# Kernel optimization log

Measured on AMD Instinct MI355X. Metric: run time of the kernel, lower is better.

Reference implementation:

```python
import jax, jax.numpy as jnp
import numpy as np

N_NODES = 100000
N_EDGES = 1600000
D_IN = 128
D_HID = 128
N_CLS = 40


def setup_inputs() -> dict:
    key = jax.random.key(0)
    ks = jax.random.split(key, 8)
    x = jax.random.normal(ks[0], (N_NODES, D_IN), dtype=jnp.float32)
    edge_index = jax.random.randint(ks[1], (2, N_EDGES), 0, N_NODES, dtype=jnp.int64)
    s = 1.0 / np.sqrt(D_IN)
    W1_l = jax.random.normal(ks[2], (D_IN, D_HID), dtype=jnp.float32) * s
    W1_r = jax.random.normal(ks[3], (D_IN, D_HID), dtype=jnp.float32) * s
    b1 = jnp.zeros((D_HID,), dtype=jnp.float32)
    s2 = 1.0 / np.sqrt(D_HID)
    W2_l = jax.random.normal(ks[4], (D_HID, N_CLS), dtype=jnp.float32) * s2
    W2_r = jax.random.normal(ks[5], (D_HID, N_CLS), dtype=jnp.float32) * s2
    b2 = jnp.zeros((N_CLS,), dtype=jnp.float32)
    return {"x": x, "edge_index": edge_index, "W1_l": W1_l, "W1_r": W1_r,
            "b1": b1, "W2_l": W2_l, "W2_r": W2_r, "b2": b2}


def _sage_conv(x, src, dst, Wl, Wr, b):
    # mean-aggregate neighbor features (PyG SAGEConv, aggr='mean')
    n = x.shape[0]
    agg = jax.ops.segment_sum(x[src], dst, num_segments=n)           # [N, d]
    deg = jax.ops.segment_sum(jnp.ones_like(dst, dtype=x.dtype), dst, num_segments=n)
    mean = agg / jnp.maximum(deg, 1.0)[:, None]
    # lin_l(mean) + bias + lin_r(x_root)  (lin_r has no bias in PyG)
    return mean @ Wl + b + x @ Wr


def reference(x, edge_index, W1_l, W1_r, b1, W2_l, W2_r, b2):
    src, dst = edge_index[0], edge_index[1]
    h = jax.nn.relu(_sage_conv(x, src, dst, W1_l, W1_r, b1))
    # F.dropout(training=...) is identity in eval mode (deterministic reference)
    out = _sage_conv(h, src, dst, W2_l, W2_r, b2)
    return jax.nn.softmax(out, axis=1)
```

## Files before the change

### kernel.cpp

```cpp
#include <hip/hip_runtime.h>

#define DIM 128
#define NCLS 40
#define CPAD 64
#define NBIN 256
#define BINSH 9
#define CHUNK 4096

typedef unsigned short ushort_t;
typedef __attribute__((ext_vector_type(8))) short bf16x8;
typedef __attribute__((ext_vector_type(4))) float f32x4;
typedef __attribute__((ext_vector_type(4))) unsigned uint4a;

__device__ __forceinline__ ushort_t f2b(float f) {
    union { float f; unsigned u; } v; v.f = f;
    unsigned r = v.u + 0x7FFFu + ((v.u >> 16) & 1u);
    return (ushort_t)(r >> 16);
}

__device__ __forceinline__ float b2f(ushort_t b) {
    union { unsigned u; float f; } v; v.u = ((unsigned)b) << 16;
    return v.f;
}

__device__ __forceinline__ void acc_fp8x4(float4& a, int w) {
    a.x += __builtin_amdgcn_cvt_f32_fp8(w, 0);
    a.y += __builtin_amdgcn_cvt_f32_fp8(w, 1);
    a.z += __builtin_amdgcn_cvt_f32_fp8(w, 2);
    a.w += __builtin_amdgcn_cvt_f32_fp8(w, 3);
}

__device__ __forceinline__ void acc_pair(float& a, float& b, unsigned u) {
    union { unsigned x; float f; } lo, hi;
    lo.x = u << 16;
    hi.x = u & 0xFFFF0000u;
    a += lo.f;
    b += hi.f;
}

__global__ __launch_bounds__(256) void prep_kernel(
    const float* __restrict__ x, ushort_t* __restrict__ xbf, unsigned* __restrict__ xq,
    const float* __restrict__ W1r, const float* __restrict__ W1l, ushort_t* __restrict__ Wp,
    const float* __restrict__ W2l, ushort_t* __restrict__ Wp2,
    int* __restrict__ binCnt, int* __restrict__ binCtr, int n4, int cb)
{
    const int b = blockIdx.x;
    if (b < cb) {
        int i = b * 256 + threadIdx.x;
        if (i >= n4) return;
        f32x4 v = __builtin_nontemporal_load(((const f32x4*)x) + i);
        ushort4 o;
        o.x = f2b(v.x); o.y = f2b(v.y); o.z = f2b(v.z); o.w = f2b(v.w);
        ((ushort4*)xbf)[i] = o;
        int p = __builtin_amdgcn_cvt_pk_fp8_f32(v.x, v.y, 0, false);
        p = __builtin_amdgcn_cvt_pk_fp8_f32(v.z, v.w, p, true);
        xq[i] = (unsigned)p;
    } else if (b < cb + 128) {
        int o = (b - cb) * 256 + threadIdx.x;
        int j    = o & 7;
        int lane = (o >> 3) & 63;
        int t    = (o >> 9) & 7;
        int kc   = o >> 12;
        int k = kc * 32 + (lane >> 4) * 8 + j;
        int nn = t * 16 + (lane & 15);
        float v = (k < DIM) ? W1r[k * DIM + nn] : W1l[(k - DIM) * DIM + nn];
        Wp[o] = f2b(v);
    } else if (b < cb + 152) {
        int o = (b - cb - 128) * 256 + threadIdx.x;
        int j    = o & 7;
        int lane = (o >> 3) & 63;
        int rem  = o >> 9;
        int t    = rem % 3;
        int kc   = rem / 3;
        int k  = kc * 32 + (lane >> 4) * 8 + j;
        int nn = t * 16 + (lane & 15);
        Wp2[o] = (nn < NCLS) ? f2b(W2l[k * NCLS + nn]) : (ushort_t)0;
    } else {
        binCnt[threadIdx.x] = 0;
        binCtr[threadIdx.x] = 0;
    }
}


__global__ __launch_bounds__(256) void bincount_kernel(const int* __restrict__ dst,
                                                       int* __restrict__ binCnt, int E) {
    __shared__ int hist[NBIN];
    hist[threadIdx.x] = 0;
    __syncthreads();
    const int tid = blockIdx.x * 256 + threadIdx.x;
    const int stride = gridDim.x * 256;
    for (int e = tid; e < E; e += stride)
        atomicAdd(&hist[__builtin_nontemporal_load(dst + e) >> BINSH], 1);
    __syncthreads();
    if (hist[threadIdx.x]) atomicAdd(&binCnt[threadIdx.x], hist[threadIdx.x]);
}

__global__ __launch_bounds__(256) void binscatter_kernel(
    const int* __restrict__ src, const int* __restrict__ dst,
    const int* __restrict__ binCnt, int* __restrict__ binCtr,
    unsigned* __restrict__ pairs, int E)
{
    __shared__ int ss[CHUNK];
    __shared__ int sd[CHUNK];
    __shared__ int excl[NBIN];
    __shared__ int hist[NBIN];
    __shared__ int base[NBIN];
    __shared__ int cnt[NBIN];
    const int t = threadIdx.x;
    excl[t] = binCnt[t];
    __syncthreads();
    for (int off = 1; off < NBIN; off <<= 1) {
        int v = (t >= off) ? excl[t - off] : 0;
        __syncthreads();
        excl[t] += v;
        __syncthreads();
    }
    const int mybase = (t == 0) ? 0 : excl[t - 1];
    __syncthreads();
    excl[t] = mybase;
    __syncthreads();
    const int nchunk = (E + CHUNK - 1) / CHUNK;
    for (int c = blockIdx.x; c < nchunk; c += gridDim.x) {
        const int e0 = c * CHUNK;
        const int m = min(CHUNK, E - e0);
        for (int i = t; i < m; i += 256) {
            ss[i] = __builtin_nontemporal_load(src + e0 + i);
            sd[i] = __builtin_nontemporal_load(dst + e0 + i);
        }
        hist[t] = 0;
        cnt[t] = 0;
        __syncthreads();
        for (int i = t; i < m; i += 256)
            atomicAdd(&hist[sd[i] >> BINSH], 1);
        __syncthreads();
        base[t] = hist[t] ? (excl[t] + atomicAdd(&binCtr[t], hist[t])) : 0;
        __syncthreads();
        for (int i = t; i < m; i += 256) {
            int d = sd[i];
            int b = d >> BINSH;
            int off = base[b] + atomicAdd(&cnt[b], 1);
            pairs[off] = ((unsigned)(d & ((1 << BINSH) - 1)) << 17) | (unsigned)ss[i];
        }
        __syncthreads();
    }
}

__global__ __launch_bounds__(256) void bincsr_kernel(
    const unsigned* __restrict__ pairs, const int* __restrict__ binCnt,
    int* __restrict__ row_ptr, int* __restrict__ eidx, int n, int E)
{
    __shared__ int bs[NBIN];
    __shared__ int deg[512];
    __shared__ int sc[512];
    __shared__ int cnt[512];
    const int b  = blockIdx.x;
    const int t = threadIdx.x;
    bs[t] = binCnt[t];
    __syncthreads();
    for (int off = 1; off < NBIN; off <<= 1) {
        int v = (t >= off) ? bs[t - off] : 0;
        __syncthreads();
        bs[t] += v;
        __syncthreads();
    }
    const int lo = (b == 0) ? 0 : bs[b - 1];
    const int hi = bs[b];
    const int nlo = b << BINSH;
    deg[t] = 0; deg[t + 256] = 0;
    cnt[t] = 0; cnt[t + 256] = 0;
    __syncthreads();
    for (int e = lo + t; e < hi; e += 256)
        atomicAdd(&deg[pairs[e] >> 17], 1);
    __syncthreads();
    sc[t] = deg[t];
    sc[t + 256] = deg[t + 256];
    __syncthreads();
    for (int off = 1; off < 512; off <<= 1) {
        int v0 = (t >= off) ? sc[t - off] : 0;
        int v1 = sc[t + 256 - off];
        __syncthreads();
        sc[t] += v0;
        sc[t + 256] += v1;
        __syncthreads();
    }
    {
        int node0 = nlo + t;
        int node1 = nlo + t + 256;
        if (node0 < n) row_ptr[node0] = lo + sc[t] - deg[t];
        if (node1 < n) row_ptr[node1] = lo + sc[t + 256] - deg[t + 256];
    }
    if (b == NBIN - 1 && t == 255) row_ptr[n] = E;
    for (int e = lo + t; e < hi; e += 256) {
        unsigned p = pairs[e];
        int dl = p >> 17;
        int slot = sc[dl] - deg[dl] + atomicAdd(&cnt[dl], 1);
        eidx[lo + slot] = (int)(p & 0x1FFFFu);
    }
}


__global__ __launch_bounds__(256) void gather128_kernel(
    const unsigned* __restrict__ xq, const int* __restrict__ row_ptr,
    const int* __restrict__ eidx, ushort_t* __restrict__ Bbf, int n)
{
    int t = blockIdx.x * 256 + threadIdx.x;
    int node = t >> 5;
    if (node >= n) return;
    int q = t & 31;
    int j  = row_ptr[node];
    int je = row_ptr[node + 1];
    const float id = 1.0f / fmaxf((float)(je - j), 1.0f);
    float4 acc = make_float4(0.f, 0.f, 0.f, 0.f);
    for (; j + 3 < je; j += 4) {
        int s0 = eidx[j], s1 = eidx[j + 1], s2 = eidx[j + 2], s3 = eidx[j + 3];
        int w0 = (int)xq[(size_t)s0 * 32 + q];
        int w1 = (int)xq[(size_t)s1 * 32 + q];
        int w2 = (int)xq[(size_t)s2 * 32 + q];
        int w3 = (int)xq[(size_t)s3 * 32 + q];
        acc_fp8x4(acc, w0); acc_fp8x4(acc, w1);
        acc_fp8x4(acc, w2); acc_fp8x4(acc, w3);
    }
    for (; j < je; ++j) {
        int s0 = eidx[j];
        acc_fp8x4(acc, (int)xq[(size_t)s0 * 32 + q]);
    }
    ushort4 o;
    o.x = f2b(acc.x * id); o.y = f2b(acc.y * id);
    o.z = f2b(acc.z * id); o.w = f2b(acc.w * id);
    ((ushort4*)(Bbf + (size_t)node * DIM))[q] = o;
}

__global__ __launch_bounds__(256) void mfma_gemm_kernel(
    const ushort_t* __restrict__ xbf, const ushort_t* __restrict__ mxbf,
    const ushort_t* __restrict__ Wp, const ushort_t* __restrict__ Wp2,
    const float* __restrict__ bias,
    ushort_t* __restrict__ Hbf, ushort_t* __restrict__ Cbf, int n)
{
    __shared__ ushort_t hl[4][16 * 136];
    const int wave = threadIdx.x >> 6;
    const int lane = threadIdx.x & 63;
    const int m16  = lane & 15;
    const int quad = lane >> 4;
    const int row0 = blockIdx.x * 64 + wave * 16;
    int arow = row0 + m16;
    if (arow >= n) arow = n - 1;
    f32x4 acc[8];
    #pragma unroll
    for (int t = 0; t < 8; ++t) acc[t] = (f32x4){0.f, 0.f, 0.f, 0.f};
    const ushort_t* __restrict__ xrow = xbf  + (size_t)arow * DIM;
    const ushort_t* __restrict__ mrow = mxbf + (size_t)arow * DIM;
    #pragma unroll
    for (int kc = 0; kc < 8; ++kc) {
        const int kcol = (kc & 3) * 32 + quad * 8;
        const bf16x8 afrag = *(const bf16x8*)((kc < 4 ? xrow : mrow) + kcol);
        const ushort_t* __restrict__ wp = Wp + (size_t)kc * 4096 + (size_t)lane * 8;
        #pragma unroll
        for (int t = 0; t < 8; ++t) {
            const bf16x8 bfrag = *(const bf16x8*)(wp + (size_t)t * 512);
            acc[t] = __builtin_amdgcn_mfma_f32_16x16x32_bf16(afrag, bfrag, acc[t], 0, 0, 0);
        }
    }
    ushort_t* __restrict__ hw = hl[wave];
    #pragma unroll
    for (int t = 0; t < 8; ++t) {
        const int col = t * 16 + m16;
        const float bv = bias[col];
        #pragma unroll
        for (int r = 0; r < 4; ++r) {
            hw[(quad * 4 + r) * 136 + col] = f2b(fmaxf(acc[t][r] + bv, 0.f));
        }
    }
    f32x4 acc2[3];
    #pragma unroll
    for (int t = 0; t < 3; ++t) acc2[t] = (f32x4){0.f, 0.f, 0.f, 0.f};
    const bool rowok = (row0 + m16) < n;
    #pragma unroll
    for (int kc = 0; kc < 4; ++kc) {
        const bf16x8 afrag2 = *(const bf16x8*)(hw + m16 * 136 + kc * 32 + quad * 8);
        if (rowok)
            *(bf16x8*)(Hbf + (size_t)(row0 + m16) * DIM + kc * 32 + quad * 8) = afrag2;
        const ushort_t* __restrict__ wp2 = Wp2 + (size_t)kc * 1536 + (size_t)lane * 8;
        #pragma unroll
        for (int t = 0; t < 3; ++t) {
            const bf16x8 bfrag = *(const bf16x8*)(wp2 + (size_t)t * 512);
            acc2[t] = __builtin_amdgcn_mfma_f32_16x16x32_bf16(afrag2, bfrag, acc2[t], 0, 0, 0);
        }
    }
    #pragma unroll
    for (int t = 0; t < 3; ++t) {
        const int col = t * 16 + m16;
        if (col >= NCLS) continue;
        #pragma unroll
        for (int r = 0; r < 4; ++r) {
            const int row = row0 + quad * 4 + r;
            if (row < n) Cbf[(size_t)row * CPAD + col] = f2b(acc2[t][r]);
        }
    }
}

__global__ __launch_bounds__(256) void final_kernel(
    const ushort_t* __restrict__ Hbf, const ushort_t* __restrict__ Cbf,
    const int* __restrict__ row_ptr, const int* __restrict__ eidx,
    const float* __restrict__ W, const float* __restrict__ b2,
    float* __restrict__ out, int n)
{
    __shared__ float lgs[64][41];
    const int tid  = threadIdx.x;
    const int q    = tid >> 6;
    const int lane = tid & 63;
    const int r    = lane & 3;
    const int na   = q * 16 + (lane >> 2);
    const int nodeA = blockIdx.x * 64 + na;
    float lg[40];
    #pragma unroll
    for (int c = 0; c < 40; ++c) lg[c] = 0.f;
    if (nodeA < n) {
        int j  = row_ptr[nodeA] + r;
        int je = row_ptr[nodeA + 1];
        for (; j < je; j += 4) {
            int s = eidx[j];
            const uint4a* __restrict__ p = (const uint4a*)(Cbf + (size_t)s * CPAD);
            uint4a v0 = p[0], v1 = p[1], v2 = p[2], v3 = p[3], v4 = p[4];
            acc_pair(lg[0],  lg[1],  v0.x); acc_pair(lg[2],  lg[3],  v0.y);
            acc_pair(lg[4],  lg[5],  v0.z); acc_pair(lg[6],  lg[7],  v0.w);
            acc_pair(lg[8],  lg[9],  v1.x); acc_pair(lg[10], lg[11], v1.y);
            acc_pair(lg[12], lg[13], v1.z); acc_pair(lg[14], lg[15], v1.w);
            acc_pair(lg[16], lg[17], v2.x); acc_pair(lg[18], lg[19], v2.y);
            acc_pair(lg[20], lg[21], v2.z); acc_pair(lg[22], lg[23], v2.w);
            acc_pair(lg[24], lg[25], v3.x); acc_pair(lg[26], lg[27], v3.y);
            acc_pair(lg[28], lg[29], v3.z); acc_pair(lg[30], lg[31], v3.w);
            acc_pair(lg[32], lg[33], v4.x); acc_pair(lg[34], lg[35], v4.y);
            acc_pair(lg[36], lg[37], v4.z); acc_pair(lg[38], lg[39], v4.w);
        }
    }
    const bool hi1 = (lane & 1) != 0;
    float h20[20];
    #pragma unroll
    for (int i = 0; i < 20; ++i) {
        float sendv = hi1 ? lg[i] : lg[20 + i];
        float recv  = __shfl_xor(sendv, 1, 64);
        h20[i] = (hi1 ? lg[20 + i] : lg[i]) + recv;
    }
    const bool hi2 = (lane & 2) != 0;
    float h10[10];
    #pragma unroll
    for (int i = 0; i < 10; ++i) {
        float sendv = hi2 ? h20[i] : h20[10 + i];
        float recv  = __shfl_xor(sendv, 2, 64);
        h10[i] = (hi2 ? h20[10 + i] : h20[i]) + recv;
    }
    const int cbase = (hi1 ? 20 : 0) + (hi2 ? 10 : 0);
    #pragma unroll
    for (int i = 0; i < 10; ++i) lgs[na][cbase + i] = h10[i];
    __syncthreads();
    const int c0 = __builtin_amdgcn_readfirstlane(q * 10);
    const int node = blockIdx.x * 64 + lane;
    if (node < n) {
        const float dg = (float)(row_ptr[node + 1] - row_ptr[node]);
        const float id = 1.0f / fmaxf(dg, 1.0f);
        float lgd[10];
        #pragma unroll
        for (int c = 0; c < 10; ++c) lgd[c] = fmaf(lgs[lane][c0 + c], id, b2[c0 + c]);
        const ushort_t* __restrict__ h = Hbf + (size_t)node * DIM;
        for (int k = 0; k < DIM; k += 4) {
            const ushort4 hu = *(const ushort4*)(h + k);
            const float hx = b2f(hu.x), hy = b2f(hu.y), hz = b2f(hu.z), hw = b2f(hu.w);
            const float* __restrict__ w0 = W + (size_t)(k + 0) * NCLS + c0;
            const float* __restrict__ w1 = W + (size_t)(k + 1) * NCLS + c0;
            const float* __restrict__ w2 = W + (size_t)(k + 2) * NCLS + c0;
            const float* __restrict__ w3 = W + (size_t)(k + 3) * NCLS + c0;
            #pragma unroll
            for (int c = 0; c < 10; ++c) {
                float a = lgd[c];
                a = fmaf(hx, w0[c], a);
                a = fmaf(hy, w1[c], a);
                a = fmaf(hz, w2[c], a);
                a = fmaf(hw, w3[c], a);
                lgd[c] = a;
            }
        }
        #pragma unroll
        for (int c = 0; c < 10; ++c) lgs[lane][c0 + c] = lgd[c];
    }
    __syncthreads();
    if (q == 0 && node < n) {
        float v[NCLS];
        #pragma unroll
        for (int c = 0; c < NCLS; ++c) v[c] = lgs[lane][c];
        float m = v[0];
        #pragma unroll
        for (int c = 1; c < NCLS; ++c) m = fmaxf(m, v[c]);
        float s = 0.f;
        #pragma unroll
        for (int c = 0; c < NCLS; ++c) { v[c] = __expf(v[c] - m); s += v[c]; }
        const float inv = 1.0f / s;
        float* __restrict__ o = out + (size_t)node * NCLS;
        #pragma unroll
        for (int c = 0; c < NCLS; ++c) o[c] = v[c] * inv;
    }
}

extern "C" void kernel_launch(void* const* d_in, const int* in_sizes, int n_in,
                              void* d_out, int out_size, void* d_ws, size_t ws_size,
                              hipStream_t stream) {
    const float* x   = (const float*)d_in[0];
    const int*   ei  = (const int*)d_in[1];
    const float* W1l = (const float*)d_in[2];
    const float* W1r = (const float*)d_in[3];
    const float* b1  = (const float*)d_in[4];
    const float* W2l = (const float*)d_in[5];
    const float* W2r = (const float*)d_in[6];
    const float* b2  = (const float*)d_in[7];
    float* out = (float*)d_out;

    const int n = in_sizes[0] / DIM;
    const int E = in_sizes[1] / 2;
    const int* src = ei;
    const int* dst = ei + E;

    ushort_t* xbf     = (ushort_t*)d_ws;
    ushort_t* mxbf    = xbf + (size_t)n * DIM;
    ushort_t* Hbf     = mxbf + (size_t)n * DIM;
    ushort_t* Cbf     = Hbf + (size_t)n * DIM;
    unsigned* xq      = (unsigned*)(Cbf + (size_t)n * CPAD);
    ushort_t* Wp      = (ushort_t*)(xq + (size_t)n * 32);
    ushort_t* Wp2     = Wp + 256 * DIM;
    int*      eidx    = (int*)(Wp2 + 4 * 1536);
    unsigned* pairs   = (unsigned*)(eidx + E);
    int*      row_ptr = (int*)(pairs + E);
    int*      binCnt  = row_ptr + (n + 1);
    int*      binCtr  = binCnt + NBIN;

    const int n4 = n * 32;
    const int cb = (n4 + 255) / 256;
    prep_kernel<<<cb + 153, 256, 0, stream>>>(x, xbf, xq, W1r, W1l, Wp,
                                              W2l, Wp2, binCnt, binCtr, n4, cb);

    bincount_kernel  <<<512, 256, 0, stream>>>(dst, binCnt, E);
    binscatter_kernel<<<512, 256, 0, stream>>>(src, dst, binCnt, binCtr, pairs, E);
    bincsr_kernel    <<<NBIN, 256, 0, stream>>>(pairs, binCnt, row_ptr, eidx, n, E);

    {
        long long t = (long long)n * 32;
        gather128_kernel<<<(int)((t + 255) / 256), 256, 0, stream>>>(xq, row_ptr, eidx, mxbf, n);
    }
    mfma_gemm_kernel<<<(n + 63) / 64, 256, 0, stream>>>(xbf, mxbf, Wp, Wp2, b1, Hbf, Cbf, n);

    final_kernel<<<(n + 63) / 64, 256, 0, stream>>>(Hbf, Cbf, row_ptr, eidx, W2r, b2, out, n);
}
```

Baseline: 302.6 us.

## Compute layer-2 root projection with MFMA in GEMM kernel, drop H round-trip

Moves the h @ W2_r projection out of the final kernel's scalar FMA loop into the MFMA GEMM kernel, using a second packed bf16 weight (Wp2r) prepared in prep_kernel. The GEMM now writes a 40-column fp32 root-term buffer instead of the full 128-wide bf16 hidden matrix, and the final kernel only adds that row. This removes per-node 128x10 scalar FMAs and the H write/read traffic, at the cost of extra MFMAs and weight loads in the GEMM and bf16 rounding of W2_r. The neighbor gather loop in the final kernel is also unrolled to two edges per iteration so more loads are in flight.

```diff
diff --git a/kernel.cpp b/kernel.cpp
--- a/kernel.cpp
+++ b/kernel.cpp
@@ -38,10 +38,25 @@
     b += hi.f;
 }
 
+__device__ __forceinline__ void acc_row40(float* lg, uint4a v0, uint4a v1,
+                                          uint4a v2, uint4a v3, uint4a v4) {
+    acc_pair(lg[0],  lg[1],  v0.x); acc_pair(lg[2],  lg[3],  v0.y);
+    acc_pair(lg[4],  lg[5],  v0.z); acc_pair(lg[6],  lg[7],  v0.w);
+    acc_pair(lg[8],  lg[9],  v1.x); acc_pair(lg[10], lg[11], v1.y);
+    acc_pair(lg[12], lg[13], v1.z); acc_pair(lg[14], lg[15], v1.w);
+    acc_pair(lg[16], lg[17], v2.x); acc_pair(lg[18], lg[19], v2.y);
+    acc_pair(lg[20], lg[21], v2.z); acc_pair(lg[22], lg[23], v2.w);
+    acc_pair(lg[24], lg[25], v3.x); acc_pair(lg[26], lg[27], v3.y);
+    acc_pair(lg[28], lg[29], v3.z); acc_pair(lg[30], lg[31], v3.w);
+    acc_pair(lg[32], lg[33], v4.x); acc_pair(lg[34], lg[35], v4.y);
+    acc_pair(lg[36], lg[37], v4.z); acc_pair(lg[38], lg[39], v4.w);
+}
+
 __global__ __launch_bounds__(256) void prep_kernel(
     const float* __restrict__ x, ushort_t* __restrict__ xbf, unsigned* __restrict__ xq,
     const float* __restrict__ W1r, const float* __restrict__ W1l, ushort_t* __restrict__ Wp,
     const float* __restrict__ W2l, ushort_t* __restrict__ Wp2,
+    const float* __restrict__ W2r, ushort_t* __restrict__ Wp2r,
     int* __restrict__ binCnt, int* __restrict__ binCtr, int n4, int cb)
 {
     const int b = blockIdx.x;
@@ -75,6 +90,16 @@
         int k  = kc * 32 + (lane >> 4) * 8 + j;
         int nn = t * 16 + (lane & 15);
         Wp2[o] = (nn < NCLS) ? f2b(W2l[k * NCLS + nn]) : (ushort_t)0;
+    } else if (b < cb + 176) {
+        int o = (b - cb - 152) * 256 + threadIdx.x;
+        int j    = o & 7;
+        int lane = (o >> 3) & 63;
+        int rem  = o >> 9;
+        int t    = rem % 3;
+        int kc   = rem / 3;
+        int k  = kc * 32 + (lane >> 4) * 8 + j;
+        int nn = t * 16 + (lane & 15);
+        Wp2r[o] = (nn < NCLS) ? f2b(W2r[k * NCLS + nn]) : (ushort_t)0;
     } else {
         binCnt[threadIdx.x] = 0;
         binCtr[threadIdx.x] = 0;
@@ -233,8 +258,8 @@
 __global__ __launch_bounds__(256) void mfma_gemm_kernel(
     const ushort_t* __restrict__ xbf, const ushort_t* __restrict__ mxbf,
     const ushort_t* __restrict__ Wp, const ushort_t* __restrict__ Wp2,
-    const float* __restrict__ bias,
-    ushort_t* __restrict__ Hbf, ushort_t* __restrict__ Cbf, int n)
+    const ushort_t* __restrict__ Wp2r, const float* __restrict__ bias,
+    ushort_t* __restrict__ Cbf, float* __restrict__ Dfl, int n)
 {
     __shared__ ushort_t hl[4][16 * 136];
     const int wave = threadIdx.x >> 6;
@@ -271,19 +296,23 @@
         }
     }
     f32x4 acc2[3];
-    #pragma unroll
-    for (int t = 0; t < 3; ++t) acc2[t] = (f32x4){0.f, 0.f, 0.f, 0.f};
-    const bool rowok = (row0 + m16) < n;
+    f32x4 acc3[3];
+    #pragma unroll
+    for (int t = 0; t < 3; ++t) {
+        acc2[t] = (f32x4){0.f, 0.f, 0.f, 0.f};
+        acc3[t] = (f32x4){0.f, 0.f, 0.f, 0.f};
+    }
     #pragma unroll
     for (int kc = 0; kc < 4; ++kc) {
         const bf16x8 afrag2 = *(const bf16x8*)(hw + m16 * 136 + kc * 32 + quad * 8);
-        if (rowok)
-            *(bf16x8*)(Hbf + (size_t)(row0 + m16) * DIM + kc * 32 + quad * 8) = afrag2;
-        const ushort_t* __restrict__ wp2 = Wp2 + (size_t)kc * 1536 + (size_t)lane * 8;
+        const ushort_t* __restrict__ wp2  = Wp2  + (size_t)kc * 1536 + (size_t)lane * 8;
+        const ushort_t* __restrict__ wp2r = Wp2r + (size_t)kc * 1536 + (size_t)lane * 8;
         #pragma unroll
         for (int t = 0; t < 3; ++t) {
-            const bf16x8 bfrag = *(const bf16x8*)(wp2 + (size_t)t * 512);
-            acc2[t] = __builtin_amdgcn_mfma_f32_16x16x32_bf16(afrag2, bfrag, acc2[t], 0, 0, 0);
+            const bf16x8 bfrag  = *(const bf16x8*)(wp2  + (size_t)t * 512);
+            const bf16x8 bfragr = *(const bf16x8*)(wp2r + (size_t)t * 512);
+            acc2[t] = __builtin_amdgcn_mfma_f32_16x16x32_bf16(afrag2, bfrag,  acc2[t], 0, 0, 0);
+            acc3[t] = __builtin_amdgcn_mfma_f32_16x16x32_bf16(afrag2, bfragr, acc3[t], 0, 0, 0);
         }
     }
     #pragma unroll
@@ -293,15 +322,18 @@
         #pragma unroll
         for (int r = 0; r < 4; ++r) {
             const int row = row0 + quad * 4 + r;
-            if (row < n) Cbf[(size_t)row * CPAD + col] = f2b(acc2[t][r]);
+            if (row < n) {
+                Cbf[(size_t)row * CPAD + col] = f2b(acc2[t][r]);
+                Dfl[(size_t)row * NCLS + col] = acc3[t][r];
+            }
         }
     }
 }
 
 __global__ __launch_bounds__(256) void final_kernel(
-    const ushort_t* __restrict__ Hbf, const ushort_t* __restrict__ Cbf,
+    const float* __restrict__ Dfl, const ushort_t* __restrict__ Cbf,
     const int* __restrict__ row_ptr, const int* __restrict__ eidx,
-    const float* __restrict__ W, const float* __restrict__ b2,
+    const float* __restrict__ b2,
     float* __restrict__ out, int n)
 {
     __shared__ float lgs[64][41];
@@ -317,20 +349,20 @@
     if (nodeA < n) {
         int j  = row_ptr[nodeA] + r;
         int je = row_ptr[nodeA + 1];
-        for (; j < je; j += 4) {
-            int s = eidx[j];
-            const uint4a* __restrict__ p = (const uint4a*)(Cbf + (size_t)s * CPAD);
-            uint4a v0 = p[0], v1 = p[1], v2 = p[2], v3 = p[3], v4 = p[4];
-            acc_pair(lg[0],  lg[1],  v0.x); acc_pair(lg[2],  lg[3],  v0.y);
-            acc_pair(lg[4],  lg[5],  v0.z); acc_pair(lg[6],  lg[7],  v0.w);
-            acc_pair(lg[8],  lg[9],  v1.x); acc_pair(lg[10], lg[11], v1.y);
-            acc_pair(lg[12], lg[13], v1.z); acc_pair(lg[14], lg[15], v1.w);
-            acc_pair(lg[16], lg[17], v2.x); acc_pair(lg[18], lg[19], v2.y);
-            acc_pair(lg[20], lg[21], v2.z); acc_pair(lg[22], lg[23], v2.w);
-            acc_pair(lg[24], lg[25], v3.x); acc_pair(lg[26], lg[27], v3.y);
-            acc_pair(lg[28], lg[29], v3.z); acc_pair(lg[30], lg[31], v3.w);
-            acc_pair(lg[32], lg[33], v4.x); acc_pair(lg[34], lg[35], v4.y);
-            acc_pair(lg[36], lg[37], v4.z); acc_pair(lg[38], lg[39], v4.w);
+        for (; j + 4 < je; j += 8) {
+            int s0 = eidx[j];
+            int s1 = eidx[j + 4];
+            const uint4a* __restrict__ p0 = (const uint4a*)(Cbf + (size_t)s0 * CPAD);
+            const uint4a* __restrict__ p1 = (const uint4a*)(Cbf + (size_t)s1 * CPAD);
+            uint4a a0 = p0[0], a1 = p0[1], a2 = p0[2], a3 = p0[3], a4 = p0[4];
+            uint4a c0v = p1[0], c1 = p1[1], c2 = p1[2], c3 = p1[3], c4 = p1[4];
+            acc_row40(lg, a0, a1, a2, a3, a4);
+            acc_row40(lg, c0v, c1, c2, c3, c4);
+        }
+        if (j < je) {
+            const uint4a* __restrict__ p0 = (const uint4a*)(Cbf + (size_t)eidx[j] * CPAD);
+            uint4a a0 = p0[0], a1 = p0[1], a2 = p0[2], a3 = p0[3], a4 = p0[4];
+            acc_row40(lg, a0, a1, a2, a3, a4);
         }
     }
     const bool hi1 = (lane & 1) != 0;
@@ -358,29 +390,10 @@
     if (node < n) {
         const float dg = (float)(row_ptr[node + 1] - row_ptr[node]);
         const float id = 1.0f / fmaxf(dg, 1.0f);
-        float lgd[10];
-        #pragma unroll
-        for (int c = 0; c < 10; ++c) lgd[c] = fmaf(lgs[lane][c0 + c], id, b2[c0 + c]);
-        const ushort_t* __restrict__ h = Hbf + (size_t)node * DIM;
-        for (int k = 0; k < DIM; k += 4) {
-            const ushort4 hu = *(const ushort4*)(h + k);
-            const float hx = b2f(hu.x), hy = b2f(hu.y), hz = b2f(hu.z), hw = b2f(hu.w);
-            const float* __restrict__ w0 = W + (size_t)(k + 0) * NCLS + c0;
-            const float* __restrict__ w1 = W + (size_t)(k + 1) * NCLS + c0;
-            const float* __restrict__ w2 = W + (size_t)(k + 2) * NCLS + c0;
-            const float* __restrict__ w3 = W + (size_t)(k + 3) * NCLS + c0;
-            #pragma unroll
-            for (int c = 0; c < 10; ++c) {
-                float a = lgd[c];
-                a = fmaf(hx, w0[c], a);
-                a = fmaf(hy, w1[c], a);
-                a = fmaf(hz, w2[c], a);
-                a = fmaf(hw, w3[c], a);
-                lgd[c] = a;
-            }
-        }
-        #pragma unroll
-        for (int c = 0; c < 10; ++c) lgs[lane][c0 + c] = lgd[c];
+        const float* __restrict__ drow = Dfl + (size_t)node * NCLS + c0;
+        #pragma unroll
+        for (int c = 0; c < 10; ++c)
+            lgs[lane][c0 + c] = fmaf(lgs[lane][c0 + c], id, b2[c0 + c]) + drow[c];
     }
     __syncthreads();
     if (q == 0 && node < n) {
@@ -420,12 +433,13 @@
 
     ushort_t* xbf     = (ushort_t*)d_ws;
     ushort_t* mxbf    = xbf + (size_t)n * DIM;
-    ushort_t* Hbf     = mxbf + (size_t)n * DIM;
-    ushort_t* Cbf     = Hbf + (size_t)n * DIM;
+    float*    Dfl     = (float*)(mxbf + (size_t)n * DIM);
+    ushort_t* Cbf     = (ushort_t*)(Dfl + (size_t)n * NCLS);
     unsigned* xq      = (unsigned*)(Cbf + (size_t)n * CPAD);
     ushort_t* Wp      = (ushort_t*)(xq + (size_t)n * 32);
     ushort_t* Wp2     = Wp + 256 * DIM;
-    int*      eidx    = (int*)(Wp2 + 4 * 1536);
+    ushort_t* Wp2r    = Wp2 + 4 * 1536;
+    int*      eidx    = (int*)(Wp2r + 4 * 1536);
     unsigned* pairs   = (unsigned*)(eidx + E);
     int*      row_ptr = (int*)(pairs + E);
     int*      binCnt  = row_ptr + (n + 1);
@@ -433,8 +447,9 @@
 
     const int n4 = n * 32;
     const int cb = (n4 + 255) / 256;
-    prep_kernel<<<cb + 153, 256, 0, stream>>>(x, xbf, xq, W1r, W1l, Wp,
-                                              W2l, Wp2, binCnt, binCtr, n4, cb);
+    prep_kernel<<<cb + 177, 256, 0, stream>>>(x, xbf, xq, W1r, W1l, Wp,
+                                              W2l, Wp2, W2r, Wp2r,
+                                              binCnt, binCtr, n4, cb);
 
     bincount_kernel  <<<512, 256, 0, stream>>>(dst, binCnt, E);
     binscatter_kernel<<<512, 256, 0, stream>>>(src, dst, binCnt, binCtr, pairs, E);
@@ -444,7 +459,8 @@
         long long t = (long long)n * 32;
         gather128_kernel<<<(int)((t + 255) / 256), 256, 0, stream>>>(xq, row_ptr, eidx, mxbf, n);
     }
-    mfma_gemm_kernel<<<(n + 63) / 64, 256, 0, stream>>>(xbf, mxbf, Wp, Wp2, b1, Hbf, Cbf, n);
-
-    final_kernel<<<(n + 63) / 64, 256, 0, stream>>>(Hbf, Cbf, row_ptr, eidx, W2r, b2, out, n);
-}
+    mfma_gemm_kernel<<<(n + 63) / 64, 256, 0, stream>>>(xbf, mxbf, Wp, Wp2, Wp2r,
+                                                        b1, Cbf, Dfl, n);
+
+    final_kernel<<<(n + 63) / 64, 256, 0, stream>>>(Dfl, Cbf, row_ptr, eidx, b2, out, n);
+}
```

New measurement: 289.6 us. -4.3%, faster.
